# Performance work log

Hardware: AMD Instinct MI355X
Metric: run time of the kernel (lower is better)

Reference implementation:

```python
import jax, jax.numpy as jnp
import numpy as np

N_SCALES = 4
EPS = 1e-8

# PyWavelets db4 decomposition filters (length 8)
_DEC_LO = np.array([-0.010597401784997278, 0.032883011666982945,
                    0.030841381835986965, -0.18703481171888114,
                    -0.02798376941698385, 0.6308807679295904,
                    0.7148465705525415, 0.23037781330885523], dtype=np.float32)
# QMF: dec_hi[n] = (-1)^(n+1) * dec_lo[L-1-n]
_DEC_HI = (_DEC_LO[::-1] * np.array([-1, 1] * 4, dtype=np.float32))
# lax.conv does cross-correlation; pywt does convolution -> reverse filters.
_KERN = np.stack([_DEC_LO[::-1], _DEC_HI[::-1]])[:, None, :]  # [2,1,8]


def _dwt1d_last(x, kern):
    """pywt single-level DWT (mode='symmetric') along the last axis.
    x: [..., N] -> (lo, hi) each [..., floor((N+L-1)/2)]."""
    L = kern.shape[-1]
    lead = x.shape[:-1]
    pad = [(0, 0)] * (x.ndim - 1) + [(L - 1, L - 1)]
    xe = jnp.pad(x, pad, mode='symmetric')[..., 1:]  # offset 1 matches pywt phase
    xb = xe.reshape(-1, 1, xe.shape[-1])
    out = jax.lax.conv_general_dilated(xb, kern, (2,), 'VALID',
                                       dimension_numbers=('NCH', 'OIH', 'NCH'))
    n_out = out.shape[-1]
    lo = out[:, 0].reshape(lead + (n_out,))
    hi = out[:, 1].reshape(lead + (n_out,))
    return lo, hi


def _dwt2(x, kern):
    """Separable 2D DWT. x: [B, H, W] -> cA, (cLH, cHL, cHH)."""
    lo, hi = _dwt1d_last(x, kern)                       # along W
    ll, lh = _dwt1d_last(jnp.swapaxes(lo, -1, -2), kern)  # along H
    hl, hh = _dwt1d_last(jnp.swapaxes(hi, -1, -2), kern)
    sw = lambda a: jnp.swapaxes(a, -1, -2)
    return sw(ll), (sw(lh), sw(hl), sw(hh))


def setup_inputs() -> dict:
    key = jax.random.key(0)
    k1, k2, k3 = jax.random.split(key, 3)
    image = jax.random.normal(k1, (16, 2, 512, 512), dtype=jnp.float32)
    t_emb = jax.random.normal(k2, (16, 64), dtype=jnp.float32)
    gate_w = jax.random.normal(k3, (64, N_SCALES), dtype=jnp.float32)
    return {"image": image, "t_emb": t_emb, "gate_w": gate_w}


def reference(image, t_emb, gate_w):
    B, C, H, W = image.shape
    kern = jnp.asarray(_KERN, dtype=image.dtype)
    x = image.reshape(B * C, H, W)

    cA = x
    mags = []  # detail magnitudes, finest first
    for _ in range(N_SCALES):
        cA, (lh, hl, hh) = _dwt2(cA, kern)
        mags.append(jnp.sqrt(lh * lh + hl * hl + hh * hh + EPS))
    mags = mags[::-1]  # coarsest first, matching pywt.wavedec2 ordering

    def up(a):  # bilinear, half-pixel centers == torch align_corners=False
        return jax.image.resize(a, (a.shape[0], H, W), 'linear')

    feats = [up(cA)] + [up(m) for m in mags]  # n_scales + 1 maps
    coarse = (feats[0] + feats[1]) * 0.5      # average cA with coarsest detail
    feats = [coarse] + feats[2:]              # n_scales maps
    wf = jnp.stack(feats, axis=1).reshape(B, C, N_SCALES, H, W)

    scale_weights = jax.nn.sigmoid(t_emb @ gate_w)  # [B, n_scales]
    wf = wf * scale_weights[:, None, :, None, None]
    return wf.reshape(B, C * N_SCALES, H, W)
```

## Files before the change

### kernel.cpp

```cpp
#include <hip/hip_runtime.h>
#include <hip/hip_bf16.h>
#include <math.h>


#define EPSV 1e-8f

__constant__ float c_lo[8] = {
    -0.010597401784997278f,  0.032883011666982945f,  0.030841381835986965f,
    -0.18703481171888114f,  -0.02798376941698385f,   0.6308807679295904f,
     0.7148465705525415f,    0.23037781330885523f };
__constant__ float c_hi[8] = {
    -0.23037781330885523f,   0.7148465705525415f,   -0.6308807679295904f,
    -0.02798376941698385f,   0.18703481171888114f,   0.030841381835986965f,
    -0.032883011666982945f, -0.010597401784997278f };

__device__ __forceinline__ int symi(int i, int n) {
    i = (i < 0) ? (-1 - i) : i;
    i = (i >= n) ? (2 * n - 1 - i) : i;
    return i;
}

template <int TO, bool AVG>
__global__ __launch_bounds__(256)
void dwt_level(const float* __restrict__ in, float* __restrict__ cA,
               float* __restrict__ mag, int N, int M, int tilesX) {
    constexpr int R = 2 * TO + 6;
    __shared__ float s_lo[R][TO + 1];
    __shared__ float s_hi[R][TO + 1];

    int T  = tilesX * tilesX;
    int n  = blockIdx.x / T;
    int t  = blockIdx.x % T;
    int tx = t % tilesX, ty = t / tilesX;
    int ox0 = tx * TO, oy0 = ty * TO;
    const float* img = in + (size_t)n * N * N;
    int qbase = 2 * oy0 - 6;

    for (int e = threadIdx.x; e < R * TO; e += 256) {
        int r = e / TO, k = e % TO;
        int gq = symi(qbase + r, N);
        const float* row = img + (size_t)gq * N;
        int base = 2 * (ox0 + k) + 1;
        float lo = 0.f, hi = 0.f;
        if (base >= 7 && base < N) {
            const float* p = row + base - 7;
#pragma unroll
            for (int j = 0; j < 8; ++j) {
                float x = p[7 - j];
                lo += c_lo[j] * x;
                hi += c_hi[j] * x;
            }
        } else {
#pragma unroll
            for (int j = 0; j < 8; ++j) {
                float x = row[symi(base - j, N)];
                lo += c_lo[j] * x;
                hi += c_hi[j] * x;
            }
        }
        s_lo[r][k] = lo;
        s_hi[r][k] = hi;
    }
    __syncthreads();

    for (int e = threadIdx.x; e < TO * TO; e += 256) {
        int ly = e / TO, k = e % TO;
        int oy = oy0 + ly, ox = ox0 + k;
        if (oy >= M || ox >= M) continue;
        float ll = 0.f, lh = 0.f, hl = 0.f, hh = 0.f;
#pragma unroll
        for (int j = 0; j < 8; ++j) {
            int r = 2 * ly + 7 - j;
            float a = s_lo[r][k];
            float b = s_hi[r][k];
            ll += c_lo[j] * a;
            lh += c_hi[j] * a;
            hl += c_lo[j] * b;
            hh += c_hi[j] * b;
        }
        size_t o = (size_t)n * M * M + (size_t)oy * M + ox;
        float m = sqrtf(lh * lh + hl * hl + hh * hh + EPSV);
        if (AVG) {
            mag[o] = 0.5f * (ll + m);
        } else {
            cA[o]  = ll;
            mag[o] = m;
        }
    }
}

#define PMAX 34
#define PSTR 35
__global__ __launch_bounds__(256)
void final_kernel(const float* __restrict__ f0,   const float* __restrict__ mag3,
                  const float* __restrict__ mag2, const float* __restrict__ mag1,
                  const float* __restrict__ t_emb, const float* __restrict__ gate_w,
                  float* __restrict__ out) {
    __shared__ float patch[PMAX * PSTR];
    __shared__ float s_sw;

    int blk  = blockIdx.x;
    int tile = blk & 63;
    int s    = (blk >> 6) & 3;
    int n    = blk >> 8;
    int b    = n >> 1, c = n & 1;
    int ti0  = (tile >> 3) * 64, tj0 = (tile & 7) * 64;

    const float* src; int ns;
    if      (s == 0) { src = f0;   ns = 38;  }
    else if (s == 1) { src = mag3; ns = 70;  }
    else if (s == 2) { src = mag2; ns = 133; }
    else             { src = mag1; ns = 259; }
    src += (size_t)n * ns * ns;
    float sc = (float)ns * (1.0f / 512.0f);

    if (threadIdx.x < 64) {
        float v = t_emb[b * 64 + threadIdx.x] * gate_w[threadIdx.x * 4 + s];
#pragma unroll
        for (int off = 32; off > 0; off >>= 1) v += __shfl_down(v, off);
        if (threadIdx.x == 0) s_sw = 1.f / (1.f + expf(-v));
    }

    int pr0 = max(0, (int)floorf(((float)ti0 + 0.5f) * sc - 0.5f));
    int pr1 = min(ns - 1, (int)floorf(((float)ti0 + 63.5f) * sc - 0.5f) + 1);
    int pc0 = max(0, (int)floorf(((float)tj0 + 0.5f) * sc - 0.5f));
    int pc1 = min(ns - 1, (int)floorf(((float)tj0 + 63.5f) * sc - 0.5f) + 1);
    int rows = pr1 - pr0 + 1, cols = pc1 - pc0 + 1;

    for (int e = threadIdx.x; e < rows * cols; e += 256) {
        int r = e / cols, cc = e % cols;
        patch[r * PSTR + cc] = src[(size_t)(pr0 + r) * ns + (pc0 + cc)];
    }
    __syncthreads();

    int tx = threadIdx.x & 15, ty = threadIdx.x >> 4;
    float sw = s_sw;

    int   j0r[4], j1r[4];
    float fjr[4];
#pragma unroll
    for (int q = 0; q < 4; ++q) {
        int j = tj0 + tx * 4 + q;
        float uj = ((float)j + 0.5f) * sc - 0.5f;
        float f0j = floorf(uj);
        int j0 = (int)f0j;
        fjr[q] = uj - f0j;
        j0r[q] = min(max(j0, 0), ns - 1) - pc0;
        j1r[q] = min(max(j0 + 1, 0), ns - 1) - pc0;
    }

    size_t obase = (((size_t)b * 8 + (c * 4 + s)) * 512) * 512;
#pragma unroll
    for (int rr = 0; rr < 4; ++rr) {
        int i = ti0 + ty + rr * 16;
        float ui = ((float)i + 0.5f) * sc - 0.5f;
        float f0i = floorf(ui);
        int i0 = (int)f0i;
        float fi = ui - f0i;
        const float* r0 = patch + (min(max(i0, 0), ns - 1) - pr0) * PSTR;
        const float* r1 = patch + (min(max(i0 + 1, 0), ns - 1) - pr0) * PSTR;
        float4 o;
        float* op = (float*)&o;
#pragma unroll
        for (int q = 0; q < 4; ++q) {
            float v00 = r0[j0r[q]], v01 = r0[j1r[q]];
            float v10 = r1[j0r[q]], v11 = r1[j1r[q]];
            float t0 = v00 + (v01 - v00) * fjr[q];
            float t1 = v10 + (v11 - v10) * fjr[q];
            op[q] = (t0 + (t1 - t0) * fi) * sw;
        }
        *(float4*)(out + obase + (size_t)i * 512 + tj0 + tx * 4) = o;
    }
}

extern "C" void kernel_launch(void* const* d_in, const int* in_sizes, int n_in,
                              void* d_out, int out_size, void* d_ws, size_t ws_size,
                              hipStream_t stream) {
    (void)in_sizes; (void)n_in; (void)out_size; (void)ws_size;
    const float* image  = (const float*)d_in[0];
    const float* t_emb  = (const float*)d_in[1];
    const float* gate_w = (const float*)d_in[2];
    float* out = (float*)d_out;
    float* ws = (float*)d_ws;

    const int NI = 32;
    const int S1 = 259 * 259, S2 = 133 * 133, S3 = 70 * 70, S4 = 38 * 38;

    size_t off = 0;
    float* mag1 = ws + off; off += (size_t)NI * S1;
    float* mag2 = ws + off; off += (size_t)NI * S2;
    float* mag3 = ws + off; off += (size_t)NI * S3;
    float* f0   = ws + off; off += (size_t)NI * S4;
    float* cA1  = ws + off; off += (size_t)NI * S1;
    float* cA2  = ws + off; off += (size_t)NI * S2;
    float* cA3  = ws + off; off += (size_t)NI * S3;

    const int TO = 32;
    auto tiles = [](int M) { return (M + TO - 1) / TO; };

    { int tX = tiles(259);
      dwt_level<TO, false><<<NI * tX * tX, 256, 0, stream>>>(image, cA1, mag1, 512, 259, tX); }
    { int tX = tiles(133);
      dwt_level<TO, false><<<NI * tX * tX, 256, 0, stream>>>(cA1, cA2, mag2, 259, 133, tX); }
    { int tX = tiles(70);
      dwt_level<TO, false><<<NI * tX * tX, 256, 0, stream>>>(cA2, cA3, mag3, 133, 70, tX); }
    { int tX = tiles(38);
      dwt_level<TO, true><<<NI * tX * tX, 256, 0, stream>>>(cA3, nullptr, f0, 70, 38, tX); }

    final_kernel<<<32 * 4 * 64, 256, 0, stream>>>(f0, mag3, mag2, mag1,
                                                  t_emb, gate_w, out);
}
```

Measured before the change: 214.5 us.

## Vectorize DWT loads/stores, pad row strides, skip edge work, nontemporal output stores

The DWT level kernel now reads input with float2 loads and computes two output columns per thread with float2 shared-memory and global stores. Odd-sized intermediate planes get even row strides (260, 134) so the paired accesses stay aligned. Edge tiles skip rows and columns beyond the valid output. The final upsampling kernel copies its patch row by row and writes the large output with nontemporal stores to avoid polluting the cache. The changes add stride bookkeeping and a vector type alias in exchange for fewer memory instructions.

```diff
diff --git a/kernel.cpp b/kernel.cpp
--- a/kernel.cpp
+++ b/kernel.cpp
@@ -1,9 +1,10 @@
 #include <hip/hip_runtime.h>
-#include <hip/hip_bf16.h>
 #include <math.h>
 
 
 #define EPSV 1e-8f
+
+typedef float f32x4 __attribute__((ext_vector_type(4)));
 
 __constant__ float c_lo[8] = {
     -0.010597401784997278f,  0.032883011666982945f,  0.030841381835986965f,
@@ -23,34 +24,39 @@
 template <int TO, bool AVG>
 __global__ __launch_bounds__(256)
 void dwt_level(const float* __restrict__ in, float* __restrict__ cA,
-               float* __restrict__ mag, int N, int M, int tilesX) {
+               float* __restrict__ mag, int N, int inStride,
+               int M, int outStride, int tilesX) {
+    static_assert(TO == 32, "TO must be 32");
     constexpr int R = 2 * TO + 6;
-    __shared__ float s_lo[R][TO + 1];
-    __shared__ float s_hi[R][TO + 1];
+    __shared__ float s_lo[R][TO + 2];
+    __shared__ float s_hi[R][TO + 2];
 
     int T  = tilesX * tilesX;
     int n  = blockIdx.x / T;
     int t  = blockIdx.x % T;
     int tx = t % tilesX, ty = t / tilesX;
     int ox0 = tx * TO, oy0 = ty * TO;
-    const float* img = in + (size_t)n * N * N;
+    const float* img = in + (size_t)n * N * inStride;
     int qbase = 2 * oy0 - 6;
-
-    for (int e = threadIdx.x; e < R * TO; e += 256) {
-        int r = e / TO, k = e % TO;
+    int kmax = min(TO, M - ox0);
+    int rmax = 2 * min(TO, M - oy0) + 6;
+
+    for (int e = threadIdx.x; e < rmax * TO; e += 256) {
+        int r = e >> 5, k = e & 31;
+        if (k >= kmax) continue;
         int gq = symi(qbase + r, N);
-        const float* row = img + (size_t)gq * N;
+        const float* row = img + (size_t)gq * inStride;
         int base = 2 * (ox0 + k) + 1;
-        float lo = 0.f, hi = 0.f;
+        float lo, hi;
         if (base >= 7 && base < N) {
-            const float* p = row + base - 7;
-#pragma unroll
-            for (int j = 0; j < 8; ++j) {
-                float x = p[7 - j];
-                lo += c_lo[j] * x;
-                hi += c_hi[j] * x;
-            }
+            const float2* p2 = (const float2*)(row + (base - 7));
+            float2 q0 = p2[0], q1 = p2[1], q2 = p2[2], q3 = p2[3];
+            lo = c_lo[0]*q3.y + c_lo[1]*q3.x + c_lo[2]*q2.y + c_lo[3]*q2.x
+               + c_lo[4]*q1.y + c_lo[5]*q1.x + c_lo[6]*q0.y + c_lo[7]*q0.x;
+            hi = c_hi[0]*q3.y + c_hi[1]*q3.x + c_hi[2]*q2.y + c_hi[3]*q2.x
+               + c_hi[4]*q1.y + c_hi[5]*q1.x + c_hi[6]*q0.y + c_hi[7]*q0.x;
         } else {
+            lo = 0.f; hi = 0.f;
 #pragma unroll
             for (int j = 0; j < 8; ++j) {
                 float x = row[symi(base - j, N)];
@@ -63,28 +69,43 @@
     }
     __syncthreads();
 
-    for (int e = threadIdx.x; e < TO * TO; e += 256) {
-        int ly = e / TO, k = e % TO;
+    for (int e = threadIdx.x; e < TO * TO / 2; e += 256) {
+        int ly = e >> 4;
+        int k  = (e & 15) * 2;
         int oy = oy0 + ly, ox = ox0 + k;
         if (oy >= M || ox >= M) continue;
-        float ll = 0.f, lh = 0.f, hl = 0.f, hh = 0.f;
+        float llx = 0.f, lly = 0.f, lhx = 0.f, lhy = 0.f;
+        float hlx = 0.f, hly = 0.f, hhx = 0.f, hhy = 0.f;
 #pragma unroll
         for (int j = 0; j < 8; ++j) {
             int r = 2 * ly + 7 - j;
-            float a = s_lo[r][k];
-            float b = s_hi[r][k];
-            ll += c_lo[j] * a;
-            lh += c_hi[j] * a;
-            hl += c_lo[j] * b;
-            hh += c_hi[j] * b;
-        }
-        size_t o = (size_t)n * M * M + (size_t)oy * M + ox;
-        float m = sqrtf(lh * lh + hl * hl + hh * hh + EPSV);
+            float2 a = *(const float2*)&s_lo[r][k];
+            float2 b = *(const float2*)&s_hi[r][k];
+            llx += c_lo[j] * a.x;  lly += c_lo[j] * a.y;
+            lhx += c_hi[j] * a.x;  lhy += c_hi[j] * a.y;
+            hlx += c_lo[j] * b.x;  hly += c_lo[j] * b.y;
+            hhx += c_hi[j] * b.x;  hhy += c_hi[j] * b.y;
+        }
+        size_t o = (size_t)n * M * outStride + (size_t)oy * outStride + ox;
+        float mx = sqrtf(lhx * lhx + hlx * hlx + hhx * hhx + EPSV);
+        float my = sqrtf(lhy * lhy + hly * hly + hhy * hhy + EPSV);
+        bool pair = (ox + 1 < M);
         if (AVG) {
-            mag[o] = 0.5f * (ll + m);
+            float fx = 0.5f * (llx + mx);
+            if (pair) {
+                float fy = 0.5f * (lly + my);
+                *(float2*)&mag[o] = make_float2(fx, fy);
+            } else {
+                mag[o] = fx;
+            }
         } else {
-            cA[o]  = ll;
-            mag[o] = m;
+            if (pair) {
+                *(float2*)&cA[o]  = make_float2(llx, lly);
+                *(float2*)&mag[o] = make_float2(mx, my);
+            } else {
+                cA[o]  = llx;
+                mag[o] = mx;
+            }
         }
     }
 }
@@ -106,12 +127,12 @@
     int b    = n >> 1, c = n & 1;
     int ti0  = (tile >> 3) * 64, tj0 = (tile & 7) * 64;
 
-    const float* src; int ns;
-    if      (s == 0) { src = f0;   ns = 38;  }
-    else if (s == 1) { src = mag3; ns = 70;  }
-    else if (s == 2) { src = mag2; ns = 133; }
-    else             { src = mag1; ns = 259; }
-    src += (size_t)n * ns * ns;
+    const float* src; int ns, st;
+    if      (s == 0) { src = f0;   ns = 38;  st = 38;  }
+    else if (s == 1) { src = mag3; ns = 70;  st = 70;  }
+    else if (s == 2) { src = mag2; ns = 133; st = 134; }
+    else             { src = mag1; ns = 259; st = 260; }
+    src += (size_t)n * ns * st;
     float sc = (float)ns * (1.0f / 512.0f);
 
     if (threadIdx.x < 64) {
@@ -127,9 +148,11 @@
     int pc1 = min(ns - 1, (int)floorf(((float)tj0 + 63.5f) * sc - 0.5f) + 1);
     int rows = pr1 - pr0 + 1, cols = pc1 - pc0 + 1;
 
-    for (int e = threadIdx.x; e < rows * cols; e += 256) {
-        int r = e / cols, cc = e % cols;
-        patch[r * PSTR + cc] = src[(size_t)(pr0 + r) * ns + (pc0 + cc)];
+    for (int r = threadIdx.x >> 5; r < rows; r += 8) {
+        const float* srow = src + (size_t)(pr0 + r) * st + pc0;
+        float* prow = patch + r * PSTR;
+        for (int cc = threadIdx.x & 31; cc < cols; cc += 32)
+            prow[cc] = srow[cc];
     }
     __syncthreads();
 
@@ -159,17 +182,16 @@
         float fi = ui - f0i;
         const float* r0 = patch + (min(max(i0, 0), ns - 1) - pr0) * PSTR;
         const float* r1 = patch + (min(max(i0 + 1, 0), ns - 1) - pr0) * PSTR;
-        float4 o;
-        float* op = (float*)&o;
+        f32x4 o;
 #pragma unroll
         for (int q = 0; q < 4; ++q) {
             float v00 = r0[j0r[q]], v01 = r0[j1r[q]];
             float v10 = r1[j0r[q]], v11 = r1[j1r[q]];
             float t0 = v00 + (v01 - v00) * fjr[q];
             float t1 = v10 + (v11 - v10) * fjr[q];
-            op[q] = (t0 + (t1 - t0) * fi) * sw;
-        }
-        *(float4*)(out + obase + (size_t)i * 512 + tj0 + tx * 4) = o;
+            o[q] = (t0 + (t1 - t0) * fi) * sw;
+        }
+        __builtin_nontemporal_store(o, (f32x4*)(out + obase + (size_t)i * 512 + tj0 + tx * 4));
     }
 }
 
@@ -184,28 +206,28 @@
     float* ws = (float*)d_ws;
 
     const int NI = 32;
-    const int S1 = 259 * 259, S2 = 133 * 133, S3 = 70 * 70, S4 = 38 * 38;
+    const int P1 = 259 * 260, P2 = 133 * 134, P3 = 70 * 70, P4 = 38 * 38;
 
     size_t off = 0;
-    float* mag1 = ws + off; off += (size_t)NI * S1;
-    float* mag2 = ws + off; off += (size_t)NI * S2;
-    float* mag3 = ws + off; off += (size_t)NI * S3;
-    float* f0   = ws + off; off += (size_t)NI * S4;
-    float* cA1  = ws + off; off += (size_t)NI * S1;
-    float* cA2  = ws + off; off += (size_t)NI * S2;
-    float* cA3  = ws + off; off += (size_t)NI * S3;
+    float* mag1 = ws + off; off += (size_t)NI * P1;
+    float* mag2 = ws + off; off += (size_t)NI * P2;
+    float* mag3 = ws + off; off += (size_t)NI * P3;
+    float* f0   = ws + off; off += (size_t)NI * P4;
+    float* cA1  = ws + off; off += (size_t)NI * P1;
+    float* cA2  = ws + off; off += (size_t)NI * P2;
+    float* cA3  = ws + off; off += (size_t)NI * P3;
 
     const int TO = 32;
     auto tiles = [](int M) { return (M + TO - 1) / TO; };
 
     { int tX = tiles(259);
-      dwt_level<TO, false><<<NI * tX * tX, 256, 0, stream>>>(image, cA1, mag1, 512, 259, tX); }
+      dwt_level<TO, false><<<NI * tX * tX, 256, 0, stream>>>(image, cA1, mag1, 512, 512, 259, 260, tX); }
     { int tX = tiles(133);
-      dwt_level<TO, false><<<NI * tX * tX, 256, 0, stream>>>(cA1, cA2, mag2, 259, 133, tX); }
+      dwt_level<TO, false><<<NI * tX * tX, 256, 0, stream>>>(cA1, cA2, mag2, 259, 260, 133, 134, tX); }
     { int tX = tiles(70);
-      dwt_level<TO, false><<<NI * tX * tX, 256, 0, stream>>>(cA2, cA3, mag3, 133, 70, tX); }
+      dwt_level<TO, false><<<NI * tX * tX, 256, 0, stream>>>(cA2, cA3, mag3, 133, 134, 70, 70, tX); }
     { int tX = tiles(38);
-      dwt_level<TO, true><<<NI * tX * tX, 256, 0, stream>>>(cA3, nullptr, f0, 70, 38, tX); }
+      dwt_level<TO, true><<<NI * tX * tX, 256, 0, stream>>>(cA3, nullptr, f0, 70, 70, 38, 38, tX); }
 
     final_kernel<<<32 * 4 * 64, 256, 0, stream>>>(f0, mag3, mag2, mag1,
                                                   t_emb, gate_w, out);
```

After: 217.2 us. No clear change (+1.3%).
